# Kernel optimization log

Hardware: AMD Instinct MI355X
Metric: run time of the kernel (lower is better)

The kernel has to match this reference:

```python
import jax, jax.numpy as jnp
import numpy as np

B, T, D = 4, 2048, 1024
H = 16            # N_HEADS
HD = D // H       # head_dim = 64
VD = 64           # VALUE_DIM


def setup_inputs() -> dict:
    key = jax.random.key(0)
    ks = jax.random.split(key, 9)
    s_in = 1.0 / np.sqrt(D)
    s_out = 1.0 / np.sqrt(H * VD)
    x = jax.random.normal(ks[0], (B, T, D), dtype=jnp.float32)
    # stacked per-head projection weights (nn.Linear applies x @ W.T; we store [in,out])
    Wq = jax.random.uniform(ks[1], (H, D, HD), jnp.float32, -s_in, s_in)
    bq = jax.random.uniform(ks[2], (H, HD), jnp.float32, -s_in, s_in)
    Wk = jax.random.uniform(ks[3], (H, D, HD), jnp.float32, -s_in, s_in)
    bk = jax.random.uniform(ks[4], (H, HD), jnp.float32, -s_in, s_in)
    Wv = jax.random.uniform(ks[5], (H, D, VD), jnp.float32, -s_in, s_in)
    bv = jax.random.uniform(ks[6], (H, VD), jnp.float32, -s_in, s_in)
    Wo = jax.random.uniform(ks[7], (H * VD, D), jnp.float32, -s_out, s_out)
    bo = jax.random.uniform(ks[8], (D,), jnp.float32, -s_out, s_out)
    return {"x": x, "Wq": Wq, "bq": bq, "Wk": Wk, "bk": bk,
            "Wv": Wv, "bv": bv, "Wo": Wo, "bo": bo}


def reference(x, Wq, bq, Wk, bk, Wv, bv, Wo, bo):
    b, t, d = x.shape
    scale = HD ** -0.5
    # per-head projections, vectorized over heads
    q = jnp.einsum('btd,hdk->bhtk', x, Wq) + bq[None, :, None, :]
    k = jnp.einsum('btd,hdk->bhtk', x, Wk) + bk[None, :, None, :]
    v = jnp.einsum('btd,hdv->bhtv', x, Wv) + bv[None, :, None, :]
    scores = jnp.einsum('bhsk,bhtk->bhst', q, k) * scale
    causal = jnp.triu(jnp.ones((t, t), dtype=bool), k=1)  # mask[i,j]=j>i
    scores = jnp.where(causal, -jnp.inf, scores)
    attn = jax.nn.softmax(scores, axis=-1)  # dropout = identity in eval
    out = jnp.einsum('bhst,bhtv->bhsv', attn, v)
    concat = out.transpose(0, 2, 1, 3).reshape(b, t, H * VD)  # cat over heads
    return concat @ Wo + bo
```

## Files before the change

### kernel.cpp

```cpp
#include <hip/hip_runtime.h>

#define Bc 4
#define Tc 2048
#define Dc 1024
#define Hc 16
#define HDc 64
#define VDc 64
#define MTOT (Bc * Tc)
#define NQKV 3072

typedef __attribute__((ext_vector_type(8))) short short8;
typedef __attribute__((ext_vector_type(4))) short short4_;
typedef __attribute__((ext_vector_type(4))) float float4_;
typedef __attribute__((ext_vector_type(4))) unsigned uint4_;

#define QSCALE 0.18033688011112042f

static __device__ __forceinline__ short f2bf(float f) {
  unsigned u = __builtin_bit_cast(unsigned, f);
  u += 0x7fffu + ((u >> 16) & 1u);
  return (short)(u >> 16);
}
static __device__ __forceinline__ unsigned packp(float a, float b) {
  unsigned ua = __builtin_bit_cast(unsigned, a) + 0x8000u;
  unsigned ub = __builtin_bit_cast(unsigned, b) + 0x8000u;
  return __builtin_amdgcn_perm(ub, ua, 0x07060302);
}

static __device__ __forceinline__ void gload16(const void* g, void* l) {
  __builtin_amdgcn_global_load_lds(
      (__attribute__((address_space(1))) void*)(unsigned long long)g,
      (__attribute__((address_space(3))) void*)l, 16, 0, 0);
}


__global__ void cvt_x_kernel(const float* __restrict__ x, short* __restrict__ xb) {
  int i = blockIdx.x * blockDim.x + threadIdx.x;
  float4_ v = reinterpret_cast<const float4_*>(x)[i];
  short4_ o;
  o[0] = f2bf(v[0]); o[1] = f2bf(v[1]); o[2] = f2bf(v[2]); o[3] = f2bf(v[3]);
  reinterpret_cast<short4_*>(xb)[i] = o;
}

__global__ __launch_bounds__(256) void build_wqkv_kernel(
    const float* __restrict__ Wq, const float* __restrict__ Wk,
    const float* __restrict__ Wv, const float* __restrict__ bq,
    const float* __restrict__ bk, const float* __restrict__ bv,
    short* __restrict__ wt, float* __restrict__ bias) {
  __shared__ __align__(16) short Lt[64][72];
  const int tid = threadIdx.x;
  const int mat = blockIdx.x >> 4, h = blockIdx.x & 15;
  const float* W  = (mat == 0) ? Wq : (mat == 1) ? Wk : Wv;
  const float* bs = (mat == 0) ? bq : (mat == 1) ? bk : bv;
  const int base_n = (mat << 10) + (h << 6);
  if (blockIdx.y == 0 && tid < 64) bias[base_n + tid] = bs[h * 64 + tid];
  for (int dc = 0; dc < 4; dc++) {
    const int d0 = blockIdx.y * 256 + dc * 64;
#pragma unroll
    for (int rep = 0; rep < 16; rep++) {
      int dl = rep * 4 + (tid >> 6);
      int hd = tid & 63;
      Lt[hd][dl] = f2bf(W[(size_t)(h * 1024 + d0 + dl) * 64 + hd]);
    }
    __syncthreads();
    int hd = tid >> 2, c = tid & 3;
    short8 v0 = *(const short8*)&Lt[hd][c * 16];
    short8 v1 = *(const short8*)&Lt[hd][c * 16 + 8];
    *(short8*)&wt[(size_t)(base_n + hd) * 1024 + d0 + c * 16] = v0;
    *(short8*)&wt[(size_t)(base_n + hd) * 1024 + d0 + c * 16 + 8] = v1;
    __syncthreads();
  }
}

__global__ __launch_bounds__(256) void build_wo_kernel(
    const float* __restrict__ Wo, short* __restrict__ wot) {
  __shared__ __align__(16) short Lt[64][72];
  const int tid = threadIdx.x;
  const int n0 = blockIdx.x * 64, k0 = blockIdx.y * 64;
#pragma unroll
  for (int rep = 0; rep < 16; rep++) {
    int kl = rep * 4 + (tid >> 6);
    int nl = tid & 63;
    Lt[nl][kl] = f2bf(Wo[(size_t)(k0 + kl) * 1024 + n0 + nl]);
  }
  __syncthreads();
  int nl = tid >> 2, c = tid & 3;
  short8 v0 = *(const short8*)&Lt[nl][c * 16];
  short8 v1 = *(const short8*)&Lt[nl][c * 16 + 8];
  *(short8*)&wot[(size_t)(n0 + nl) * 1024 + k0 + c * 16] = v0;
  *(short8*)&wot[(size_t)(n0 + nl) * 1024 + k0 + c * 16 + 8] = v1;
}

#define GEMM_KLOOP(SHSZ)                                                       \
  __shared__ __align__(16) short Sh[SHSZ];                                     \
  const int tid = threadIdx.x;                                                 \
  const int wave = tid >> 6, lane = tid & 63;                                  \
  const int lm = lane & 15, quad = lane >> 4;                                  \
  const int wm = (wave & 1) * 64, wn = (wave >> 1) * 64;                       \
  const int srow = tid >> 2, pchunk = tid & 3;                                 \
  const int swr = (srow ^ (srow >> 2)) & 3;                                    \
  const int pq = quad ^ ((lm ^ (lm >> 2)) & 3);                                \
  const short* Ag = A + (size_t)(m0 + srow) * 1024 + (pchunk ^ swr) * 8;       \
  const short* Bg = Bt + (size_t)(n0 + srow) * 1024 + (pchunk ^ swr) * 8;      \
  float4_ acc[4][4] = {};                                                      \
  gload16(Ag, &Sh[wave * 512]);                                                \
  gload16(Ag + 64 * 1024, &Sh[2048 + wave * 512]);                             \
  gload16(Bg, &Sh[4096 + wave * 512]);                                         \
  gload16(Bg + 64 * 1024, &Sh[6144 + wave * 512]);                             \
  for (int k0 = 0; k0 < 1024; k0 += 32) {                                      \
    const int cb = (k0 >> 5) & 1;                                              \
    __syncthreads();                                                           \
    if (k0 + 32 < 1024) {                                                      \
      short* d = &Sh[(1 - cb) * 8192];                                         \
      gload16(Ag + k0 + 32, d + wave * 512);                                   \
      gload16(Ag + 64 * 1024 + k0 + 32, d + 2048 + wave * 512);                \
      gload16(Bg + k0 + 32, d + 4096 + wave * 512);                            \
      gload16(Bg + 64 * 1024 + k0 + 32, d + 6144 + wave * 512);                \
    }                                                                          \
    const short* Ab = &Sh[cb * 8192];                                          \
    const short* Bb = &Sh[cb * 8192 + 4096];                                   \
    short8 af[4], bf[4];                                                       \
    _Pragma("unroll") for (int i = 0; i < 4; i++) {                            \
      af[i] = *(const short8*)&Ab[(wm + i * 16 + lm) * 32 + pq * 8];           \
      bf[i] = *(const short8*)&Bb[(wn + i * 16 + lm) * 32 + pq * 8];           \
    }                                                                          \
    _Pragma("unroll") for (int i = 0; i < 4; i++)                              \
      _Pragma("unroll") for (int j = 0; j < 4; j++)                            \
        acc[i][j] = __builtin_amdgcn_mfma_f32_16x16x32_bf16(af[i], bf[j],      \
                                                            acc[i][j], 0, 0, 0); \
  }

__global__ __launch_bounds__(256) void gemm_qkv_kernel(
    const short* __restrict__ A, const short* __restrict__ Bt,
    const float* __restrict__ bias,
    short* __restrict__ Qb, short* __restrict__ Kb, short* __restrict__ Vt) {
  const int m0 = blockIdx.x * 128, n0 = blockIdx.y * 128;
  GEMM_KLOOP(18432)
  __syncthreads();
  short* epi = &Sh[wave * 4608];
  const int mat = n0 >> 10;
  const int hh = ((n0 + wn) >> 6) & 15;
  const int b = m0 >> 11;
  const int bh = b * Hc + hh;
  const int t0 = (m0 & (Tc - 1)) + wm;
  if (mat < 2) {
    const float sc = (mat == 0) ? QSCALE : 1.0f;
#pragma unroll
    for (int j = 0; j < 4; j++) {
      float bvs = bias[n0 + wn + j * 16 + lm] * sc;
#pragma unroll
      for (int i = 0; i < 4; i++)
#pragma unroll
        for (int r = 0; r < 4; r++)
          epi[(i * 16 + quad * 4 + r) * 72 + j * 16 + lm] = f2bf(acc[i][j][r] * sc + bvs);
    }
    __asm__ volatile("s_waitcnt lgkmcnt(0)" ::: "memory");
    short* dst = (mat == 0) ? Qb : Kb;
#pragma unroll
    for (int p = 0; p < 8; p++) {
      int lrow = p * 8 + (lane >> 3);
      short8 v = *(const short8*)&epi[lrow * 72 + (lane & 7) * 8];
      *(short8*)&dst[((size_t)bh * Tc + t0 + lrow) * HDc + (lane & 7) * 8] = v;
    }
  } else {
#pragma unroll
    for (int j = 0; j < 4; j++) {
      float bv = bias[n0 + wn + j * 16 + lm];
#pragma unroll
      for (int i = 0; i < 4; i++) {
        short4_ pk;
#pragma unroll
        for (int r = 0; r < 4; r++) pk[r] = f2bf(acc[i][j][r] + bv);
        *(short4_*)&epi[(j * 16 + lm) * 72 + i * 16 + quad * 4] = pk;
      }
    }
    __asm__ volatile("s_waitcnt lgkmcnt(0)" ::: "memory");
#pragma unroll
    for (int p = 0; p < 8; p++) {
      int hdrow = p * 8 + (lane >> 3);
      short8 v = *(const short8*)&epi[hdrow * 72 + (lane & 7) * 8];
      *(short8*)&Vt[((size_t)bh * VDc + hdrow) * Tc + t0 + (lane & 7) * 8] = v;
    }
  }
}

__global__ __launch_bounds__(256) void gemm_out_kernel(
    const short* __restrict__ A, const short* __restrict__ Bt,
    const float* __restrict__ bo, float* __restrict__ out) {
  const int m0 = blockIdx.x * 128, n0 = blockIdx.y * 128;
  GEMM_KLOOP(16384)
#pragma unroll
  for (int j = 0; j < 4; j++) {
    int n = n0 + wn + j * 16 + lm;
    float bv = bo[n];
#pragma unroll
    for (int i = 0; i < 4; i++) {
#pragma unroll
      for (int r = 0; r < 4; r++) {
        int m = m0 + wm + i * 16 + quad * 4 + r;
        out[(size_t)m * Dc + n] = acc[i][j][r] + bv;
      }
    }
  }
}

__global__ __launch_bounds__(256, 2) void attn_kernel(
    const short* __restrict__ Qb, const short* __restrict__ Kb,
    const short* __restrict__ Vt, short* __restrict__ AO) {
  __shared__ __align__(16) short Sh[16384];
  const int tid = threadIdx.x;
  const int wave = tid >> 6, lane = tid & 63;
  const int lm = lane & 15, quad = lane >> 4;
  const int bh = blockIdx.y;
  const int qblk = (blockIdx.y < 32) ? (7 - blockIdx.x) : blockIdx.x;
  const int q0 = qblk * 256 + wave * 64;

  const short* Qp = Qb + (size_t)bh * Tc * HDc;
  const short* Kp = Kb + (size_t)bh * Tc * HDc;
  const short* Vp = Vt + (size_t)bh * VDc * Tc;

  const int srow = tid >> 3;
  const int chlog = (tid & 7) ^ (srow & 7);
  const int sw = lm & 7;

  short8 qf[4][2];
#pragma unroll
  for (int g = 0; g < 4; g++)
#pragma unroll
    for (int h = 0; h < 2; h++)
      qf[g][h] = *(const short8*)&Qp[(q0 + g * 16 + lm) * HDc + h * 32 + quad * 8];

  float4_ o[4][4] = {};
  float lsum[4] = {};
  unsigned pk[4][4][2];

  const int nt = 4 * qblk + 4;
#pragma unroll
  for (int c = 0; c < 2; c++) {
    gload16(Kp + (size_t)(c * 32 + srow) * HDc + chlog * 8, &Sh[c * 2048 + wave * 512]);
    gload16(Vp + (size_t)(c * 32 + srow) * Tc + chlog * 8, &Sh[8192 + c * 2048 + wave * 512]);
  }

  for (int it = 0; it < nt; ++it) {
    const int kt = it << 6;
    const int cur = it & 1;
    __syncthreads();
    if (it + 1 < nt) {
      const int ktn = kt + 64;
      const int nb = (1 - cur) * 4096;
#pragma unroll
      for (int c = 0; c < 2; c++) {
        gload16(Kp + (size_t)(ktn + c * 32 + srow) * HDc + chlog * 8, &Sh[nb + c * 2048 + wave * 512]);
        gload16(Vp + (size_t)(c * 32 + srow) * Tc + ktn + chlog * 8, &Sh[8192 + nb + c * 2048 + wave * 512]);
      }
    }
    if (kt > q0 + 63) continue;
    const short* Kt = &Sh[cur * 4096];
    const short* Vtl = &Sh[8192 + cur * 4096];
    const bool diag = (kt + 63 > q0);

#pragma unroll
    for (int mf = 0; mf < 4; ++mf) {
      int row = mf * 16 + lm;
      short8 k0 = *(const short8*)&Kt[row * 64 + (quad ^ sw) * 8];
      short8 k1 = *(const short8*)&Kt[row * 64 + ((4 + quad) ^ sw) * 8];
      float4_ st[4];
#pragma unroll
      for (int g = 0; g < 4; ++g) {
        float4_ s = {};
        s = __builtin_amdgcn_mfma_f32_16x16x32_bf16(k0, qf[g][0], s, 0, 0, 0);
        s = __builtin_amdgcn_mfma_f32_16x16x32_bf16(k1, qf[g][1], s, 0, 0, 0);
        st[g] = s;
      }
      if (diag) {
#pragma unroll
        for (int g = 0; g < 4; ++g) {
          int qrow = q0 + g * 16 + lm;
#pragma unroll
          for (int r = 0; r < 4; ++r)
            if (kt + mf * 16 + quad * 4 + r > qrow) st[g][r] = -1e30f;
        }
      }
#pragma unroll
      for (int g = 0; g < 4; ++g) {
        float p0 = __builtin_amdgcn_exp2f(st[g][0]);
        float p1 = __builtin_amdgcn_exp2f(st[g][1]);
        float p2 = __builtin_amdgcn_exp2f(st[g][2]);
        float p3 = __builtin_amdgcn_exp2f(st[g][3]);
        lsum[g] += (p0 + p1) + (p2 + p3);
        pk[mf][g][0] = packp(p0, p1);
        pk[mf][g][1] = packp(p2, p3);
      }
    }

#pragma unroll
    for (int h = 0; h < 2; ++h) {
      short8 bfr[4];
#pragma unroll
      for (int g = 0; g < 4; ++g) {
        uint4_ bu = {pk[2 * h][g][0], pk[2 * h][g][1], pk[2 * h + 1][g][0], pk[2 * h + 1][g][1]};
        bfr[g] = __builtin_bit_cast(short8, bu);
      }
#pragma unroll
      for (int mf2 = 0; mf2 < 4; ++mf2) {
        int row = mf2 * 16 + lm;
        short4_ va = *(const short4_*)&Vtl[row * 64 + ((4 * h + (quad >> 1)) ^ sw) * 8 + (quad & 1) * 4];
        short4_ vb = *(const short4_*)&Vtl[row * 64 + ((4 * h + 2 + (quad >> 1)) ^ sw) * 8 + (quad & 1) * 4];
        short8 af = __builtin_shufflevector(va, vb, 0, 1, 2, 3, 4, 5, 6, 7);
#pragma unroll
        for (int g = 0; g < 4; ++g)
          o[mf2][g] = __builtin_amdgcn_mfma_f32_16x16x32_bf16(af, bfr[g], o[mf2][g], 0, 0, 0);
      }
    }
  }

  float inv[4];
#pragma unroll
  for (int g = 0; g < 4; ++g) {
    float s = lsum[g];
    s += __shfl_xor(s, 16);
    s += __shfl_xor(s, 32);
    inv[g] = 1.0f / s;
  }

  __syncthreads();
  const int b = bh >> 4, h = bh & 15;
  short* epi = &Sh[wave * 4096];
#pragma unroll
  for (int g = 0; g < 4; ++g) {
#pragma unroll
    for (int mf2 = 0; mf2 < 4; ++mf2) {
      short4_ pkv;
      pkv[0] = f2bf(o[mf2][g][0] * inv[g]); pkv[1] = f2bf(o[mf2][g][1] * inv[g]);
      pkv[2] = f2bf(o[mf2][g][2] * inv[g]); pkv[3] = f2bf(o[mf2][g][3] * inv[g]);
      *(short4_*)&epi[(g * 16 + lm) * 64 + ((2 * mf2 + (quad >> 1)) ^ sw) * 8 + (quad & 1) * 4] = pkv;
    }
  }
  __asm__ volatile("s_waitcnt lgkmcnt(0)" ::: "memory");
#pragma unroll
  for (int p = 0; p < 8; ++p) {
    int lr = p * 8 + (lane >> 3);
    short8 vv = *(const short8*)&epi[lr * 64 + ((lane & 7) ^ (lr & 7)) * 8];
    *(short8*)&AO[((size_t)(b * Tc + q0 + lr)) * 1024 + h * 64 + (lane & 7) * 8] = vv;
  }
}

extern "C" void kernel_launch(void* const* d_in, const int* in_sizes, int n_in,
                              void* d_out, int out_size, void* d_ws, size_t ws_size,
                              hipStream_t stream) {
  const float* x  = (const float*)d_in[0];
  const float* Wq = (const float*)d_in[1];
  const float* bq = (const float*)d_in[2];
  const float* Wk = (const float*)d_in[3];
  const float* bk = (const float*)d_in[4];
  const float* Wv = (const float*)d_in[5];
  const float* bv = (const float*)d_in[6];
  const float* Wo = (const float*)d_in[7];
  const float* bo = (const float*)d_in[8];
  float* out = (float*)d_out;

  char* ws = (char*)d_ws;
  size_t off = 0;
  short* xb   = (short*)(ws + off); off += (size_t)MTOT * Dc * 2;
  short* wqkv = (short*)(ws + off); off += (size_t)NQKV * Dc * 2;
  float* bqkv = (float*)(ws + off); off += ((size_t)NQKV * 4 + 255) & ~255ull;
  short* Qb   = (short*)(ws + off); off += (size_t)Bc * Hc * Tc * HDc * 2;
  short* Kb   = (short*)(ws + off); off += (size_t)Bc * Hc * Tc * HDc * 2;
  short* Vt   = (short*)(ws + off); off += (size_t)Bc * Hc * VDc * Tc * 2;
  short* AO   = (short*)(ws + off); off += (size_t)MTOT * 1024 * 2;
  short* wot  = (short*)(ws + off); off += (size_t)Dc * Dc * 2;

  cvt_x_kernel<<<MTOT * Dc / (256 * 4), 256, 0, stream>>>(x, xb);
  build_wqkv_kernel<<<dim3(48, 4), 256, 0, stream>>>(Wq, Wk, Wv, bq, bk, bv, wqkv, bqkv);
  build_wo_kernel<<<dim3(16, 16), 256, 0, stream>>>(Wo, wot);
  gemm_qkv_kernel<<<dim3(MTOT / 128, NQKV / 128), 256, 0, stream>>>(xb, wqkv, bqkv, Qb, Kb, Vt);
  attn_kernel<<<dim3(8, Bc * Hc), 256, 0, stream>>>(Qb, Kb, Vt, AO);
  gemm_out_kernel<<<dim3(MTOT / 128, Dc / 128), 256, 0, stream>>>(AO, wot, bo, out);
}
```

Baseline: 252.2 us.

## Rewrite QKV GEMM with 256x256 tiles, 8 waves, swizzled LDS and interleaved prefetch

```diff
diff --git a/kernel.cpp b/kernel.cpp
--- a/kernel.cpp
+++ b/kernel.cpp
@@ -130,56 +130,148 @@
                                                             acc[i][j], 0, 0, 0); \
   }
 
-__global__ __launch_bounds__(256) void gemm_qkv_kernel(
+#define LG0 asm volatile("s_waitcnt lgkmcnt(0)")
+#define BARRIER do { asm volatile("" ::: "memory"); __builtin_amdgcn_s_barrier(); asm volatile("" ::: "memory"); } while (0)
+
+#define LDA4(DST, MOFF)                                                        \
+  _Pragma("unroll") for (int mi = 0; mi < 4; ++mi) {                           \
+    DST[mi][0] = *(const short8*)(Ar + (MOFF + mi) * 1024 + s0v);              \
+    DST[mi][1] = *(const short8*)(Ar + (MOFF + mi) * 1024 + (s0v ^ 32));       \
+  }
+#define LDB2(DST, NOFF)                                                        \
+  _Pragma("unroll") for (int nj = 0; nj < 2; ++nj) {                           \
+    DST[nj][0] = *(const short8*)(Br + (NOFF + nj) * 1024 + s0v);              \
+    DST[nj][1] = *(const short8*)(Br + (NOFF + nj) * 1024 + (s0v ^ 32));       \
+  }
+#define MF16(AF, BF, MO, NO)                                                   \
+  _Pragma("unroll") for (int mi = 0; mi < 4; ++mi)                             \
+  _Pragma("unroll") for (int nj = 0; nj < 2; ++nj) {                           \
+    acc[MO + mi][NO + nj] = __builtin_amdgcn_mfma_f32_16x16x32_bf16(           \
+        AF[mi][0], BF[nj][0], acc[MO + mi][NO + nj], 0, 0, 0);                 \
+    acc[MO + mi][NO + nj] = __builtin_amdgcn_mfma_f32_16x16x32_bf16(           \
+        AF[mi][1], BF[nj][1], acc[MO + mi][NO + nj], 0, 0, 0);                 \
+  }
+
+#define TILE(T, DOB, DOA, VMWAIT) {                                            \
+  const short* Ar = &Sh[((T) & 1) * 16384 + wr * 8192 + lm * 64];              \
+  const short* Br = &Sh[32768 + ((T) & 1) * 16384 + (wc >> 1) * 8192 +         \
+                        (wc & 1) * 4096 + lm * 64];                            \
+  short8 af[4][2], bfa[2][2], bfb[2][2];                                       \
+  LDA4(af, 0) LDB2(bfa, 0)                                                     \
+  if (DOB) { stB((T) + 1, 0); stB((T) + 1, 1); }                               \
+  BARRIER; LG0;                                                                \
+  __builtin_amdgcn_s_setprio(1); MF16(af, bfa, 0, 0)                           \
+  __builtin_amdgcn_s_setprio(0); BARRIER;                                      \
+  LDB2(bfb, 2)                                                                 \
+  BARRIER; LG0;                                                                \
+  __builtin_amdgcn_s_setprio(1); MF16(af, bfb, 0, 2)                           \
+  __builtin_amdgcn_s_setprio(0); BARRIER;                                      \
+  LDA4(af, 4)                                                                  \
+  BARRIER; LG0;                                                                \
+  __builtin_amdgcn_s_setprio(1); MF16(af, bfb, 4, 2)                           \
+  __builtin_amdgcn_s_setprio(0); BARRIER;                                      \
+  if (DOA) { stA((T) + 2, 0); stA((T) + 2, 1); }                               \
+  __builtin_amdgcn_s_setprio(1); MF16(af, bfa, 4, 0)                           \
+  __builtin_amdgcn_s_setprio(0);                                               \
+  VMWAIT;                                                                      \
+  BARRIER; }
+
+__global__ __launch_bounds__(512, 2) void gemm_qkv_kernel(
     const short* __restrict__ A, const short* __restrict__ Bt,
     const float* __restrict__ bias,
     short* __restrict__ Qb, short* __restrict__ Kb, short* __restrict__ Vt) {
-  const int m0 = blockIdx.x * 128, n0 = blockIdx.y * 128;
-  GEMM_KLOOP(18432)
-  __syncthreads();
-  short* epi = &Sh[wave * 4608];
+  __shared__ __align__(16) short Sh[65536];
+  const int tid = threadIdx.x;
+  const int w = tid >> 6, lane = tid & 63;
+  const int lm = lane & 15, quad = lane >> 4;
+  const int wr = w >> 2, wc = w & 3;
+  const int m0 = blockIdx.x * 256, n0 = blockIdx.y * 256;
+
+  const int r0 = w * 16 + (lane >> 3);
+  const int c8 = ((lane & 7) ^ (lane >> 3)) * 8;
+  const short* Ag = A + (size_t)m0 * 1024 + c8;
+  const short* Bg = Bt + (size_t)n0 * 1024 + c8;
+  const int s0v = (quad ^ (lm & 7)) * 8;
+
+  float4_ acc[8][4] = {};
+
+  auto stA = [&](int kt, int h) {
+    const short* g = Ag + (size_t)(h * 128 + r0) * 1024 + kt * 64;
+    short* d = (short*)&Sh[(kt & 1) * 16384 + h * 8192 + w * 1024];
+    gload16(g, d);
+    gload16(g + 8 * 1024, d + 512);
+  };
+  auto stB = [&](int kt, int h) {
+    const short* g = Bg + (size_t)(h * 128 + r0) * 1024 + kt * 64;
+    short* d = (short*)&Sh[32768 + (kt & 1) * 16384 + h * 8192 + w * 1024];
+    gload16(g, d);
+    gload16(g + 8 * 1024, d + 512);
+  };
+
+  stA(0, 0); stA(0, 1); stB(0, 0); stB(0, 1); stA(1, 0); stA(1, 1);
+  asm volatile("s_waitcnt vmcnt(4)" ::: "memory");
+  __builtin_amdgcn_s_barrier();
+  asm volatile("" ::: "memory");
+
+  for (int t = 0; t < 14; ++t)
+    TILE(t, 1, 1, asm volatile("s_waitcnt vmcnt(4)" ::: "memory"))
+  TILE(14, 1, 0, asm volatile("s_waitcnt vmcnt(0)" ::: "memory"))
+  TILE(15, 0, 0, (void)0)
+
   const int mat = n0 >> 10;
-  const int hh = ((n0 + wn) >> 6) & 15;
+  const int hh = ((n0 >> 6) + wc) & 15;
   const int b = m0 >> 11;
   const int bh = b * Hc + hh;
-  const int t0 = (m0 & (Tc - 1)) + wm;
+  const int t0 = (m0 & (Tc - 1)) + wr * 128;
+  short* epi = (short*)&Sh[w * 8192];
+
   if (mat < 2) {
     const float sc = (mat == 0) ? QSCALE : 1.0f;
 #pragma unroll
-    for (int j = 0; j < 4; j++) {
-      float bvs = bias[n0 + wn + j * 16 + lm] * sc;
-#pragma unroll
-      for (int i = 0; i < 4; i++)
-#pragma unroll
-        for (int r = 0; r < 4; r++)
-          epi[(i * 16 + quad * 4 + r) * 72 + j * 16 + lm] = f2bf(acc[i][j][r] * sc + bvs);
-    }
-    __asm__ volatile("s_waitcnt lgkmcnt(0)" ::: "memory");
+    for (int nj = 0; nj < 4; ++nj) {
+      float bvs = bias[n0 + wc * 64 + nj * 16 + lm] * sc;
+#pragma unroll
+      for (int mi = 0; mi < 8; ++mi)
+#pragma unroll
+        for (int r = 0; r < 4; ++r) {
+          int row = mi * 16 + quad * 4 + r;
+          int chunk = nj * 2 + (lm >> 3);
+          epi[row * 64 + ((chunk ^ (row & 7)) << 3) + (lm & 7)] =
+              f2bf(acc[mi][nj][r] * sc + bvs);
+        }
+    }
+    asm volatile("s_waitcnt lgkmcnt(0)" ::: "memory");
     short* dst = (mat == 0) ? Qb : Kb;
 #pragma unroll
-    for (int p = 0; p < 8; p++) {
-      int lrow = p * 8 + (lane >> 3);
-      short8 v = *(const short8*)&epi[lrow * 72 + (lane & 7) * 8];
-      *(short8*)&dst[((size_t)bh * Tc + t0 + lrow) * HDc + (lane & 7) * 8] = v;
+    for (int p = 0; p < 16; ++p) {
+      int lr = p * 8 + (lane >> 3);
+      int cc = lane & 7;
+      short8 v = *(const short8*)&epi[lr * 64 + ((cc ^ (lr & 7)) << 3)];
+      *(short8*)&dst[((size_t)bh * Tc + t0 + lr) * HDc + cc * 8] = v;
     }
   } else {
 #pragma unroll
-    for (int j = 0; j < 4; j++) {
-      float bv = bias[n0 + wn + j * 16 + lm];
-#pragma unroll
-      for (int i = 0; i < 4; i++) {
-        short4_ pk;
-#pragma unroll
-        for (int r = 0; r < 4; r++) pk[r] = f2bf(acc[i][j][r] + bv);
-        *(short4_*)&epi[(j * 16 + lm) * 72 + i * 16 + quad * 4] = pk;
-      }
-    }
-    __asm__ volatile("s_waitcnt lgkmcnt(0)" ::: "memory");
-#pragma unroll
-    for (int p = 0; p < 8; p++) {
-      int hdrow = p * 8 + (lane >> 3);
-      short8 v = *(const short8*)&epi[hdrow * 72 + (lane & 7) * 8];
-      *(short8*)&Vt[((size_t)bh * VDc + hdrow) * Tc + t0 + (lane & 7) * 8] = v;
+    for (int nj = 0; nj < 4; ++nj) {
+      float bv = bias[n0 + wc * 64 + nj * 16 + lm];
+#pragma unroll
+      for (int mi = 0; mi < 8; ++mi) {
+        short4_ pk4;
+#pragma unroll
+        for (int r = 0; r < 4; ++r) pk4[r] = f2bf(acc[mi][nj][r] + bv);
+        int vd = nj * 16 + lm;
+        int tcw = mi * 2 + (quad >> 1);
+        int pos = (tcw & 8) | ((tcw ^ vd) & 7);
+        *(short4_*)&epi[vd * 128 + (pos << 3) + ((quad & 1) << 2)] = pk4;
+      }
+    }
+    asm volatile("s_waitcnt lgkmcnt(0)" ::: "memory");
+#pragma unroll
+    for (int p = 0; p < 16; ++p) {
+      int vr = p * 4 + (lane >> 4);
+      int tc = lane & 15;
+      int pos = (tc & 8) | ((tc ^ vr) & 7);
+      short8 v = *(const short8*)&epi[vr * 128 + (pos << 3)];
+      *(short8*)&Vt[((size_t)bh * VDc + vr) * Tc + t0 + tc * 8] = v;
     }
   }
 }
@@ -373,7 +465,7 @@
   cvt_x_kernel<<<MTOT * Dc / (256 * 4), 256, 0, stream>>>(x, xb);
   build_wqkv_kernel<<<dim3(48, 4), 256, 0, stream>>>(Wq, Wk, Wv, bq, bk, bv, wqkv, bqkv);
   build_wo_kernel<<<dim3(16, 16), 256, 0, stream>>>(Wo, wot);
-  gemm_qkv_kernel<<<dim3(MTOT / 128, NQKV / 128), 256, 0, stream>>>(xb, wqkv, bqkv, Qb, Kb, Vt);
+  gemm_qkv_kernel<<<dim3(MTOT / 256, NQKV / 256), 512, 0, stream>>>(xb, wqkv, bqkv, Qb, Kb, Vt);
   attn_kernel<<<dim3(8, Bc * Hc), 256, 0, stream>>>(Qb, Kb, Vt, AO);
   gemm_out_kernel<<<dim3(MTOT / 128, Dc / 128), 256, 0, stream>>>(AO, wot, bo, out);
 }
```

After: 250.7 us. About the same (-0.6%).
